# Optimization experiments

Measured on AMD Instinct MI355X. Metric: run time of the kernel, lower is better.

Reference implementation:

```python
import jax, jax.numpy as jnp
import numpy as np

N, E, G = 50000, 800000, 128
F_IN, H, NHID, C = 310, 128, 64, 2  # H = 2*nhid
NEG_SLOPE = 0.2


def setup_inputs() -> dict:
    key = jax.random.key(0)
    ks = jax.random.split(key, 16)
    def lin(k, fan_in, shape):
        return (jax.random.normal(k, shape, jnp.float32) / np.sqrt(fan_in)).astype(jnp.float32)
    return {
        "x": jax.random.normal(ks[0], (N, F_IN), jnp.float32),
        "edge_index": jax.random.randint(ks[1], (2, E), 0, N, dtype=jnp.int32),
        "batch": jnp.sort(jax.random.randint(ks[2], (N,), 0, G, dtype=jnp.int32)),
        "W1": lin(ks[3], F_IN, (F_IN, H)),
        "a_src1": lin(ks[4], H, (H,)),
        "a_dst1": lin(ks[5], H, (H,)),
        "b1": jnp.zeros((H,), jnp.float32),
        "W2": lin(ks[6], H, (H, H)),
        "a_src2": lin(ks[7], H, (H,)),
        "a_dst2": lin(ks[8], H, (H,)),
        "b2": jnp.zeros((H,), jnp.float32),
        "fc1_w": lin(ks[9], H, (H, NHID)),
        "fc1_b": jnp.zeros((NHID,), jnp.float32),
        "fc2_w": lin(ks[10], NHID, (NHID, C)),
        "fc2_b": jnp.zeros((C,), jnp.float32),
    }


def _gat(x, src, dst, W, a_src, a_dst, b):
    # PyG GATConv, heads=1: h = xW; e_ij = LeakyReLU(a_src.h_j + a_dst.h_i)
    h = x @ W                               # [N, H]
    asrc = h @ a_src                        # [N]
    adst = h @ a_dst                        # [N]
    e = jax.nn.leaky_relu(asrc[src] + adst[dst], NEG_SLOPE)  # [E']
    # segment softmax over incoming edges of each target node
    m = jax.ops.segment_max(e, dst, num_segments=N)
    ex = jnp.exp(e - m[dst])
    s = jax.ops.segment_sum(ex, dst, num_segments=N)
    w = ex / s[dst]                         # [E']
    out = jax.ops.segment_sum(h[src] * w[:, None], dst, num_segments=N)
    return out + b


def reference(x, edge_index, batch, W1, a_src1, a_dst1, b1,
              W2, a_src2, a_dst2, b2, fc1_w, fc1_b, fc2_w, fc2_b):
    # add self loops (GATConv default add_self_loops=True)
    ar = jnp.arange(N, dtype=edge_index.dtype)
    src = jnp.concatenate([edge_index[0], ar])
    dst = jnp.concatenate([edge_index[1], ar])

    h = jax.nn.selu(_gat(x, src, dst, W1, a_src1, a_dst1, b1))
    h = jax.nn.selu(_gat(h, src, dst, W2, a_src2, a_dst2, b2))

    # global mean pool over graphs
    summed = jax.ops.segment_sum(h, batch, num_segments=G)          # [G, H]
    cnt = jax.ops.segment_sum(jnp.ones((N,), h.dtype), batch, num_segments=G)
    pooled = jax.nn.selu(summed / jnp.maximum(cnt, 1.0)[:, None])

    z = jax.nn.selu(pooled @ fc1_w + fc1_b)  # dropout is identity in eval
    logits = z @ fc2_w + fc2_b
    return jax.nn.log_softmax(logits, axis=-1)
```

## Files before the change

kernel.cpp:

```cpp
#include <hip/hip_runtime.h>
#include <hip/hip_bf16.h>
#include <math.h>

#define NN 50000
#define NE 800000
#define NET (NE + NN)
#define FIN 310
#define HD 128
#define NHID 64
#define NCLS 2
#define NG 128
#define NEG_SLOPE 0.2f
#define KP1 320
#define KP2 128

#define SLOTS 64
#define NPART 8
#define PART_SZ (NN / NPART)
#define EPB 4096
#define NSLICE ((NET + EPB - 1) / EPB)

#define SELU_SCALE 1.0507009873554804934193349852946f
#define SELU_ALPHA 1.6732632423543772848170429916717f

typedef short bf16x8 __attribute__((ext_vector_type(8)));
typedef float f32x4 __attribute__((ext_vector_type(4)));

__device__ __forceinline__ float selu(float x) {
    return SELU_SCALE * (x > 0.f ? x : SELU_ALPHA * (__expf(x) - 1.f));
}
__device__ __forceinline__ float lrelu(float x) {
    return x > 0.f ? x : NEG_SLOPE * x;
}
__device__ __forceinline__ unsigned short f2bf(float f) {
    unsigned int u = __float_as_uint(f);
    u = (u + 0x7fffu + ((u >> 16) & 1u)) >> 16;
    return (unsigned short)u;
}
__device__ __forceinline__ float bf2f(unsigned short b) {
    return __uint_as_float(((unsigned int)b) << 16);
}


__global__ __launch_bounds__(256) void k_scatter_slots(const int* __restrict__ ei,
                                                       int* __restrict__ cursor,
                                                       int* __restrict__ slots) {
    int part = blockIdx.x & (NPART - 1);
    int slice = blockIdx.x >> 3;
    int lo = part * PART_SZ;
    int base = slice * EPB + threadIdx.x;
#pragma unroll
    for (int k = 0; k < EPB / 256; ++k) {
        int i = base + k * 256;
        if (i >= NET) break;
        int d = (i < NE) ? ei[NE + i] : (i - NE);
        if ((unsigned)(d - lo) < (unsigned)PART_SZ) {
            int s = (i < NE) ? ei[i] : d;
            int pos = atomicAdd(&cursor[d], 1) & (SLOTS - 1);
            slots[(size_t)d * SLOTS + pos] = s;
        }
    }
}


__global__ void k_castT2(const float* __restrict__ W1, const float* __restrict__ W2,
                         unsigned short* __restrict__ W1t, unsigned short* __restrict__ W2t) {
    int i = blockIdx.x * blockDim.x + threadIdx.x;
    const int N1 = HD * KP1;
    if (i < N1) {
        int n = i / KP1, k = i % KP1;
        W1t[i] = (k < FIN) ? f2bf(W1[(size_t)k * HD + n]) : (unsigned short)0;
    } else {
        int j = i - N1;
        if (j < HD * KP2) {
            int n = j / KP2, k = j % KP2;
            W2t[j] = f2bf(W2[(size_t)k * HD + n]);
        }
    }
}


#define GEMM_EPILOGUE                                                          \
    int rh = w & 1, chf = w >> 1;                                              \
    int gr_base = r0 + rh * 16 + quad * 4;                                     \
    _Pragma("unroll")                                                          \
    for (int r = 0; r < 4; ++r) {                                              \
        int gr = gr_base + r;                                                  \
        if (gr < M) {                                                          \
            _Pragma("unroll")                                                  \
            for (int nt = 0; nt < 4; ++nt)                                     \
                C[(size_t)gr * HD + chf * 64 + nt * 16 + l16] = f2bf(acc[nt][r]); \
        }                                                                      \
    }                                                                          \
    _Pragma("unroll")                                                          \
    for (int r = 0; r < 4; ++r) {                                              \
        float s1 = 0.f, s2 = 0.f;                                              \
        _Pragma("unroll")                                                      \
        for (int nt = 0; nt < 4; ++nt) {                                       \
            int c = chf * 64 + nt * 16 + l16;                                  \
            float v = acc[nt][r];                                              \
            s1 += v * a1s[c];                                                  \
            s2 += v * a2s[c];                                                  \
        }                                                                      \
        _Pragma("unroll")                                                      \
        for (int off = 1; off < 16; off <<= 1) {                               \
            s1 += __shfl_xor(s1, off);                                         \
            s2 += __shfl_xor(s2, off);                                         \
        }                                                                      \
        if (l16 == 0) {                                                        \
            pd[0][rh][chf][quad * 4 + r] = s1;                                 \
            pd[1][rh][chf][quad * 4 + r] = s2;                                 \
        }                                                                      \
    }                                                                          \
    __syncthreads();                                                           \
    if (t < 64) {                                                              \
        int idx = t & 15;                                                      \
        int rh2 = (t >> 4) & 1;                                                \
        int which = t >> 5;                                                    \
        float val = pd[which][rh2][0][idx] + pd[which][rh2][1][idx];           \
        int gr = r0 + rh2 * 16 + idx;                                          \
        if (gr < M) { if (which) adstp[gr] = val; else asrcp[gr] = val; }      \
    }

__global__ __launch_bounds__(256) void k_gemm_f32(const float* __restrict__ A,
                                                  const unsigned short* __restrict__ Bt,
                                                  unsigned short* __restrict__ C,
                                                  float* __restrict__ asrcp,
                                                  float* __restrict__ adstp,
                                                  const float* __restrict__ a_src,
                                                  const float* __restrict__ a_dst,
                                                  int M, int K, int Kp) {
    __shared__ unsigned short As[32][40];
    __shared__ unsigned short Bs[128][40];
    __shared__ float a1s[HD], a2s[HD];
    __shared__ float pd[2][2][2][16];
    int t = threadIdx.x;
    int lane = t & 63, w = t >> 6;
    int quad = lane >> 4, l16 = lane & 15;
    int r0 = blockIdx.x * 32;

    if (t < HD) a1s[t] = a_src[t];
    else a2s[t - HD] = a_dst[t - HD];

    f32x4 acc[4] = {};
    int arow = t >> 4;
    int acol = (t & 15) * 2;
    int brow = t >> 1;
    int bcol = (t & 1) * 16;

    for (int k0 = 0; k0 < Kp; k0 += 32) {
#pragma unroll
        for (int p = 0; p < 2; ++p) {
            int rl = arow + p * 16;
            int gr = r0 + rl;
            int gk = k0 + acol;
            float2 v = make_float2(0.f, 0.f);
            if (gr < M) {
                if (gk + 1 < K) v = *(const float2*)(A + (size_t)gr * K + gk);
                else if (gk < K) v.x = A[(size_t)gr * K + gk];
            }
            ushort2 b;
            b.x = f2bf(v.x); b.y = f2bf(v.y);
            *(ushort2*)&As[rl][acol] = b;
        }
        {
            const unsigned short* src = Bt + (size_t)brow * Kp + k0 + bcol;
            uint4 u0 = *(const uint4*)(src);
            uint4 u1 = *(const uint4*)(src + 8);
            *(uint4*)&Bs[brow][bcol] = u0;
            *(uint4*)&Bs[brow][bcol + 8] = u1;
        }
        __syncthreads();
        bf16x8 af = *(bf16x8*)&As[(w & 1) * 16 + l16][quad * 8];
#pragma unroll
        for (int nt = 0; nt < 4; ++nt) {
            bf16x8 bfr = *(bf16x8*)&Bs[(w >> 1) * 64 + nt * 16 + l16][quad * 8];
            acc[nt] = __builtin_amdgcn_mfma_f32_16x16x32_bf16(af, bfr, acc[nt], 0, 0, 0);
        }
        __syncthreads();
    }
    GEMM_EPILOGUE
}

__global__ __launch_bounds__(256) void k_gemm_bf16(const unsigned short* __restrict__ A,
                                                   const unsigned short* __restrict__ Bt,
                                                   unsigned short* __restrict__ C,
                                                   float* __restrict__ asrcp,
                                                   float* __restrict__ adstp,
                                                   const float* __restrict__ a_src,
                                                   const float* __restrict__ a_dst,
                                                   int M, int K, int Kp) {
    __shared__ unsigned short As[32][40];
    __shared__ unsigned short Bs[128][40];
    __shared__ float a1s[HD], a2s[HD];
    __shared__ float pd[2][2][2][16];
    int t = threadIdx.x;
    int lane = t & 63, w = t >> 6;
    int quad = lane >> 4, l16 = lane & 15;
    int r0 = blockIdx.x * 32;

    if (t < HD) a1s[t] = a_src[t];
    else a2s[t - HD] = a_dst[t - HD];

    f32x4 acc[4] = {};
    int arow = t >> 3;
    int acol = (t & 7) * 4;
    int brow = t >> 1;
    int bcol = (t & 1) * 16;

    for (int k0 = 0; k0 < Kp; k0 += 32) {
        {
            int gr = r0 + arow;
            uint2 v = make_uint2(0, 0);
            if (gr < M) v = *(const uint2*)(A + (size_t)gr * K + k0 + acol);
            *(uint2*)&As[arow][acol] = v;
        }
        {
            const unsigned short* src = Bt + (size_t)brow * Kp + k0 + bcol;
            uint4 u0 = *(const uint4*)(src);
            uint4 u1 = *(const uint4*)(src + 8);
            *(uint4*)&Bs[brow][bcol] = u0;
            *(uint4*)&Bs[brow][bcol + 8] = u1;
        }
        __syncthreads();
        bf16x8 af = *(bf16x8*)&As[(w & 1) * 16 + l16][quad * 8];
#pragma unroll
        for (int nt = 0; nt < 4; ++nt) {
            bf16x8 bfr = *(bf16x8*)&Bs[(w >> 1) * 64 + nt * 16 + l16][quad * 8];
            acc[nt] = __builtin_amdgcn_mfma_f32_16x16x32_bf16(af, bfr, acc[nt], 0, 0, 0);
        }
        __syncthreads();
    }
    GEMM_EPILOGUE
}


__global__ __launch_bounds__(256) void k_gat(const unsigned short* __restrict__ h,
                                             const float* __restrict__ asrc,
                                             const float* __restrict__ adst,
                                             const int* __restrict__ degv,
                                             const int* __restrict__ slots,
                                             const float* __restrict__ bias,
                                             unsigned short* __restrict__ out) {
    int node = blockIdx.x * 4 + (threadIdx.x >> 6);
    int lane = threadIdx.x & 63;
    if (node >= NN) return;
    int g = lane >> 4, cl = lane & 15;
    int deg = degv[node];
    float adsti = adst[node];

    float2 acc2[4] = {};

    int cnt = min(deg, SLOTS);
    int s_c = 0; float p_c = 0.f;
    if (lane < cnt) {
        s_c = slots[(size_t)node * SLOTS + lane];
        p_c = __expf(lrelu(asrc[s_c] + adsti));
    }
    float den_l = p_c;
    int nt = (cnt + 3) >> 2;
    for (int t = 0; t < nt; t += 2) {
        float pv[2]; uint4 hv[2];
#pragma unroll
        for (int u = 0; u < 2; ++u) {
            int tt = t + u;
            bool valid = tt < nt;
            int e = (4 * tt + g) & 63;
            int s = __shfl(s_c, e);
            float p = __shfl(p_c, e);
            int sa = valid ? s : 0;
            pv[u] = valid ? p : 0.f;
            hv[u] = *(const uint4*)(h + (size_t)sa * HD + cl * 8);
        }
#pragma unroll
        for (int u = 0; u < 2; ++u) {
            float p = pv[u];
            unsigned int w0 = hv[u].x, w1 = hv[u].y, w2 = hv[u].z, w3 = hv[u].w;
            acc2[0].x += p * __uint_as_float(w0 << 16);
            acc2[0].y += p * __uint_as_float(w0 & 0xffff0000u);
            acc2[1].x += p * __uint_as_float(w1 << 16);
            acc2[1].y += p * __uint_as_float(w1 & 0xffff0000u);
            acc2[2].x += p * __uint_as_float(w2 << 16);
            acc2[2].y += p * __uint_as_float(w2 & 0xffff0000u);
            acc2[3].x += p * __uint_as_float(w3 << 16);
            acc2[3].y += p * __uint_as_float(w3 & 0xffff0000u);
        }
    }
#pragma unroll
    for (int k = 0; k < 4; ++k) {
        acc2[k].x += __shfl_xor(acc2[k].x, 16);
        acc2[k].y += __shfl_xor(acc2[k].y, 16);
        acc2[k].x += __shfl_xor(acc2[k].x, 32);
        acc2[k].y += __shfl_xor(acc2[k].y, 32);
    }
#pragma unroll
    for (int off = 32; off; off >>= 1)
        den_l += __shfl_xor(den_l, off);

    if (g == 0) {
        float inv = 1.f / den_l;
        int c0 = cl * 8;
        float4 b0 = *(const float4*)(bias + c0);
        float4 b1 = *(const float4*)(bias + c0 + 4);
        float v0 = selu(acc2[0].x * inv + b0.x);
        float v1 = selu(acc2[0].y * inv + b0.y);
        float v2 = selu(acc2[1].x * inv + b0.z);
        float v3 = selu(acc2[1].y * inv + b0.w);
        float v4 = selu(acc2[2].x * inv + b1.x);
        float v5 = selu(acc2[2].y * inv + b1.y);
        float v6 = selu(acc2[3].x * inv + b1.z);
        float v7 = selu(acc2[3].y * inv + b1.w);
        uint4 pk;
        pk.x = (unsigned int)f2bf(v0) | ((unsigned int)f2bf(v1) << 16);
        pk.y = (unsigned int)f2bf(v2) | ((unsigned int)f2bf(v3) << 16);
        pk.z = (unsigned int)f2bf(v4) | ((unsigned int)f2bf(v5) << 16);
        pk.w = (unsigned int)f2bf(v6) | ((unsigned int)f2bf(v7) << 16);
        *(uint4*)(out + (size_t)node * HD + c0) = pk;
    }
}


__device__ __forceinline__ int lower_bound_i(const int* a, int n, int key) {
    int lo = 0, hi = n;
    while (lo < hi) {
        int mid = (lo + hi) >> 1;
        if (a[mid] < key) lo = mid + 1; else hi = mid;
    }
    return lo;
}

__global__ __launch_bounds__(512) void k_poolfc(const unsigned short* __restrict__ x,
                                                const int* __restrict__ batch,
                                                const float* __restrict__ w1,
                                                const float* __restrict__ b1,
                                                const float* __restrict__ w2,
                                                const float* __restrict__ b2,
                                                float* __restrict__ out) {
    int g = blockIdx.x;
    int t = threadIdx.x;
    __shared__ int lo_s, hi_s;
    __shared__ float red[512];
    __shared__ float pooled_s[128];
    if (t == 0) {
        lo_s = lower_bound_i(batch, NN, g);
        hi_s = lower_bound_i(batch, NN, g + 1);
    }
    __syncthreads();
    int lo = lo_s, hi = hi_s;
    float acc = 0.f;
    for (int n = lo + (t >> 7); n < hi; n += 4)
        acc += bf2f(x[(size_t)n * HD + (t & 127)]);
    red[t] = acc;
    __syncthreads();
    if (t < 128) {
        float v = red[t] + red[t + 128] + red[t + 256] + red[t + 384];
        pooled_s[t] = selu(v / fmaxf((float)(hi - lo), 1.f));
    }
    __syncthreads();
    if (t < 64) {
        float z = 0.f;
#pragma unroll 8
        for (int k = 0; k < HD; ++k) z += pooled_s[k] * w1[k * NHID + t];
        z = selu(z + b1[t]);
        float p0 = z * w2[t * NCLS + 0];
        float p1 = z * w2[t * NCLS + 1];
        for (int off = 32; off; off >>= 1) {
            p0 += __shfl_down(p0, off);
            p1 += __shfl_down(p1, off);
        }
        if (t == 0) {
            float l0 = p0 + b2[0], l1 = p1 + b2[1];
            float m = fmaxf(l0, l1);
            float lse = m + __logf(__expf(l0 - m) + __expf(l1 - m));
            out[g * NCLS + 0] = l0 - lse;
            out[g * NCLS + 1] = l1 - lse;
        }
    }
}


static inline size_t align_up(size_t v, size_t a) { return (v + a - 1) / a * a; }

extern "C" void kernel_launch(void* const* d_in, const int* in_sizes, int n_in,
                              void* d_out, int out_size, void* d_ws, size_t ws_size,
                              hipStream_t stream) {
    const float* x      = (const float*)d_in[0];
    const int*   ei     = (const int*)d_in[1];
    const int*   batch  = (const int*)d_in[2];
    const float* W1     = (const float*)d_in[3];
    const float* a_src1 = (const float*)d_in[4];
    const float* a_dst1 = (const float*)d_in[5];
    const float* b1     = (const float*)d_in[6];
    const float* W2     = (const float*)d_in[7];
    const float* a_src2 = (const float*)d_in[8];
    const float* a_dst2 = (const float*)d_in[9];
    const float* b2     = (const float*)d_in[10];
    const float* fc1_w  = (const float*)d_in[11];
    const float* fc1_b  = (const float*)d_in[12];
    const float* fc2_w  = (const float*)d_in[13];
    const float* fc2_b  = (const float*)d_in[14];
    float* out = (float*)d_out;

    char* ws = (char*)d_ws;
    size_t off = 0;
    unsigned short* h1 = (unsigned short*)(ws + off); off = align_up(off + (size_t)NN * HD * 2, 256);
    unsigned short* o1 = (unsigned short*)(ws + off); off = align_up(off + (size_t)NN * HD * 2, 256);
    float* asrc = (float*)(ws + off); off = align_up(off + (size_t)NN * 4, 256);
    float* adst = (float*)(ws + off); off = align_up(off + (size_t)NN * 4, 256);
    int* cursor = (int*)(ws + off);   off = align_up(off + (size_t)NN * 4, 256);
    int* slots  = (int*)(ws + off);   off = align_up(off + (size_t)NN * SLOTS * 4, 256);
    unsigned short* W1t = (unsigned short*)(ws + off); off = align_up(off + (size_t)HD * KP1 * 2, 256);
    unsigned short* W2t = (unsigned short*)(ws + off); off = align_up(off + (size_t)HD * KP2 * 2, 256);
    (void)ws_size;

    hipMemsetAsync(cursor, 0, (size_t)NN * 4, stream);
    k_scatter_slots<<<NSLICE * NPART, 256, 0, stream>>>(ei, cursor, slots);

    k_castT2<<<(HD * (KP1 + KP2) + 255) / 256, 256, 0, stream>>>(W1, W2, W1t, W2t);

    int gblocks = (NN + 31) / 32;

    k_gemm_f32<<<gblocks, 256, 0, stream>>>(x, W1t, h1, asrc, adst, a_src1, a_dst1, NN, FIN, KP1);
    k_gat<<<(NN + 3) / 4, 256, 0, stream>>>(h1, asrc, adst, cursor, slots, b1, o1);

    k_gemm_bf16<<<gblocks, 256, 0, stream>>>(o1, W2t, h1, asrc, adst, a_src2, a_dst2, NN, HD, KP2);
    k_gat<<<(NN + 3) / 4, 256, 0, stream>>>(h1, asrc, adst, cursor, slots, b2, o1);

    k_poolfc<<<NG, 512, 0, stream>>>(o1, batch, fc1_w, fc1_b, fc2_w, fc2_b, out);
}
```

Baseline: 309.1 us.

## Rewrite GEMMs to read pre-cast bf16 operands directly from global memory without LDS

Adds a separate pass that casts x to padded bf16 and repacks the weights into an MFMA-fragment-friendly layout. The two GEMM kernels are merged into one templated kernel that loads A and B fragments straight from global memory, with no shared-memory staging or barriers, and computes 64 rows by 128 columns per block. It also shrinks the slot-list indices from int to 16-bit. The new cast pass adds an extra write and read of x, and the 16-bit indices cannot hold node ids of 65536 or more, but NN is 50000.

New measurement: 314.1 us. Within noise of the previous version (+1.6%).

```diff
diff --git a/kernel.cpp b/kernel.cpp
--- a/kernel.cpp
+++ b/kernel.cpp
@@ -44,7 +44,7 @@
 
 __global__ __launch_bounds__(256) void k_scatter_slots(const int* __restrict__ ei,
                                                        int* __restrict__ cursor,
-                                                       int* __restrict__ slots) {
+                                                       unsigned short* __restrict__ slots) {
     int part = blockIdx.x & (NPART - 1);
     int slice = blockIdx.x >> 3;
     int lo = part * PART_SZ;
@@ -57,181 +57,103 @@
         if ((unsigned)(d - lo) < (unsigned)PART_SZ) {
             int s = (i < NE) ? ei[i] : d;
             int pos = atomicAdd(&cursor[d], 1) & (SLOTS - 1);
-            slots[(size_t)d * SLOTS + pos] = s;
-        }
-    }
-}
-
-
-__global__ void k_castT2(const float* __restrict__ W1, const float* __restrict__ W2,
-                         unsigned short* __restrict__ W1t, unsigned short* __restrict__ W2t) {
+            slots[(size_t)d * SLOTS + pos] = (unsigned short)s;
+        }
+    }
+}
+
+
+__global__ __launch_bounds__(256) void k_castx(const float* __restrict__ x,
+                                               unsigned short* __restrict__ xbf) {
+    int i = blockIdx.x * blockDim.x + threadIdx.x;
+    if (i >= NN * (KP1 / 2)) return;
+    int row = i / (KP1 / 2);
+    int kk = (i % (KP1 / 2)) * 2;
+    unsigned int pk = 0;
+    if (kk + 1 < FIN) {
+        float2 v = *(const float2*)(x + (size_t)row * FIN + kk);
+        pk = (unsigned int)f2bf(v.x) | ((unsigned int)f2bf(v.y) << 16);
+    }
+    *(unsigned int*)(xbf + (size_t)row * KP1 + kk) = pk;
+}
+
+
+__global__ void k_castW(const float* __restrict__ W1, const float* __restrict__ W2,
+                        unsigned short* __restrict__ W1p, unsigned short* __restrict__ W2p) {
     int i = blockIdx.x * blockDim.x + threadIdx.x;
     const int N1 = HD * KP1;
     if (i < N1) {
         int n = i / KP1, k = i % KP1;
-        W1t[i] = (k < FIN) ? f2bf(W1[(size_t)k * HD + n]) : (unsigned short)0;
+        unsigned short v = (k < FIN) ? f2bf(W1[(size_t)k * HD + n]) : (unsigned short)0;
+        W1p[((k >> 3) * HD + n) * 8 + (k & 7)] = v;
     } else {
         int j = i - N1;
         if (j < HD * KP2) {
             int n = j / KP2, k = j % KP2;
-            W2t[j] = f2bf(W2[(size_t)k * HD + n]);
-        }
-    }
-}
-
-
-#define GEMM_EPILOGUE                                                          \
-    int rh = w & 1, chf = w >> 1;                                              \
-    int gr_base = r0 + rh * 16 + quad * 4;                                     \
-    _Pragma("unroll")                                                          \
-    for (int r = 0; r < 4; ++r) {                                              \
-        int gr = gr_base + r;                                                  \
-        if (gr < M) {                                                          \
-            _Pragma("unroll")                                                  \
-            for (int nt = 0; nt < 4; ++nt)                                     \
-                C[(size_t)gr * HD + chf * 64 + nt * 16 + l16] = f2bf(acc[nt][r]); \
-        }                                                                      \
-    }                                                                          \
-    _Pragma("unroll")                                                          \
-    for (int r = 0; r < 4; ++r) {                                              \
-        float s1 = 0.f, s2 = 0.f;                                              \
-        _Pragma("unroll")                                                      \
-        for (int nt = 0; nt < 4; ++nt) {                                       \
-            int c = chf * 64 + nt * 16 + l16;                                  \
-            float v = acc[nt][r];                                              \
-            s1 += v * a1s[c];                                                  \
-            s2 += v * a2s[c];                                                  \
-        }                                                                      \
-        _Pragma("unroll")                                                      \
-        for (int off = 1; off < 16; off <<= 1) {                               \
-            s1 += __shfl_xor(s1, off);                                         \
-            s2 += __shfl_xor(s2, off);                                         \
-        }                                                                      \
-        if (l16 == 0) {                                                        \
-            pd[0][rh][chf][quad * 4 + r] = s1;                                 \
-            pd[1][rh][chf][quad * 4 + r] = s2;                                 \
-        }                                                                      \
-    }                                                                          \
-    __syncthreads();                                                           \
-    if (t < 64) {                                                              \
-        int idx = t & 15;                                                      \
-        int rh2 = (t >> 4) & 1;                                                \
-        int which = t >> 5;                                                    \
-        float val = pd[which][rh2][0][idx] + pd[which][rh2][1][idx];           \
-        int gr = r0 + rh2 * 16 + idx;                                          \
-        if (gr < M) { if (which) adstp[gr] = val; else asrcp[gr] = val; }      \
-    }
-
-__global__ __launch_bounds__(256) void k_gemm_f32(const float* __restrict__ A,
-                                                  const unsigned short* __restrict__ Bt,
-                                                  unsigned short* __restrict__ C,
-                                                  float* __restrict__ asrcp,
-                                                  float* __restrict__ adstp,
-                                                  const float* __restrict__ a_src,
-                                                  const float* __restrict__ a_dst,
-                                                  int M, int K, int Kp) {
-    __shared__ unsigned short As[32][40];
-    __shared__ unsigned short Bs[128][40];
-    __shared__ float a1s[HD], a2s[HD];
-    __shared__ float pd[2][2][2][16];
+            W2p[((k >> 3) * HD + n) * 8 + (k & 7)] = f2bf(W2[(size_t)k * HD + n]);
+        }
+    }
+}
+
+
+template <int KP>
+__global__ __launch_bounds__(256) void k_gemm(const unsigned short* __restrict__ A,
+                                              const unsigned short* __restrict__ Bp,
+                                              unsigned short* __restrict__ C,
+                                              float* __restrict__ asrcp,
+                                              float* __restrict__ adstp,
+                                              const float* __restrict__ a_src,
+                                              const float* __restrict__ a_dst,
+                                              int M) {
     int t = threadIdx.x;
     int lane = t & 63, w = t >> 6;
     int quad = lane >> 4, l16 = lane & 15;
-    int r0 = blockIdx.x * 32;
-
-    if (t < HD) a1s[t] = a_src[t];
-    else a2s[t - HD] = a_dst[t - HD];
-
-    f32x4 acc[4] = {};
-    int arow = t >> 4;
-    int acol = (t & 15) * 2;
-    int brow = t >> 1;
-    int bcol = (t & 1) * 16;
-
-    for (int k0 = 0; k0 < Kp; k0 += 32) {
-#pragma unroll
-        for (int p = 0; p < 2; ++p) {
-            int rl = arow + p * 16;
-            int gr = r0 + rl;
-            int gk = k0 + acol;
-            float2 v = make_float2(0.f, 0.f);
-            if (gr < M) {
-                if (gk + 1 < K) v = *(const float2*)(A + (size_t)gr * K + gk);
-                else if (gk < K) v.x = A[(size_t)gr * K + gk];
-            }
-            ushort2 b;
-            b.x = f2bf(v.x); b.y = f2bf(v.y);
-            *(ushort2*)&As[rl][acol] = b;
-        }
-        {
-            const unsigned short* src = Bt + (size_t)brow * Kp + k0 + bcol;
-            uint4 u0 = *(const uint4*)(src);
-            uint4 u1 = *(const uint4*)(src + 8);
-            *(uint4*)&Bs[brow][bcol] = u0;
-            *(uint4*)&Bs[brow][bcol + 8] = u1;
-        }
-        __syncthreads();
-        bf16x8 af = *(bf16x8*)&As[(w & 1) * 16 + l16][quad * 8];
-#pragma unroll
-        for (int nt = 0; nt < 4; ++nt) {
-            bf16x8 bfr = *(bf16x8*)&Bs[(w >> 1) * 64 + nt * 16 + l16][quad * 8];
+    int r0 = blockIdx.x * 64;
+
+    int grow = r0 + w * 16 + l16;
+    int arow = min(grow, M - 1);
+    const unsigned short* aptr = A + (size_t)arow * KP + quad * 8;
+
+    f32x4 acc[8] = {};
+#pragma unroll 2
+    for (int k0 = 0; k0 < KP; k0 += 32) {
+        bf16x8 af = *(const bf16x8*)(aptr + k0);
+        const unsigned short* bbase = Bp + ((size_t)(k0 >> 3) + quad) * (HD * 8) + l16 * 8;
+#pragma unroll
+        for (int nt = 0; nt < 8; ++nt) {
+            bf16x8 bfr = *(const bf16x8*)(bbase + nt * 128);
             acc[nt] = __builtin_amdgcn_mfma_f32_16x16x32_bf16(af, bfr, acc[nt], 0, 0, 0);
         }
-        __syncthreads();
-    }
-    GEMM_EPILOGUE
-}
-
-__global__ __launch_bounds__(256) void k_gemm_bf16(const unsigned short* __restrict__ A,
-                                                   const unsigned short* __restrict__ Bt,
-                                                   unsigned short* __restrict__ C,
-                                                   float* __restrict__ asrcp,
-                                                   float* __restrict__ adstp,
-                                                   const float* __restrict__ a_src,
-                                                   const float* __restrict__ a_dst,
-                                                   int M, int K, int Kp) {
-    __shared__ unsigned short As[32][40];
-    __shared__ unsigned short Bs[128][40];
-    __shared__ float a1s[HD], a2s[HD];
-    __shared__ float pd[2][2][2][16];
-    int t = threadIdx.x;
-    int lane = t & 63, w = t >> 6;
-    int quad = lane >> 4, l16 = lane & 15;
-    int r0 = blockIdx.x * 32;
-
-    if (t < HD) a1s[t] = a_src[t];
-    else a2s[t - HD] = a_dst[t - HD];
-
-    f32x4 acc[4] = {};
-    int arow = t >> 3;
-    int acol = (t & 7) * 4;
-    int brow = t >> 1;
-    int bcol = (t & 1) * 16;
-
-    for (int k0 = 0; k0 < Kp; k0 += 32) {
-        {
-            int gr = r0 + arow;
-            uint2 v = make_uint2(0, 0);
-            if (gr < M) v = *(const uint2*)(A + (size_t)gr * K + k0 + acol);
-            *(uint2*)&As[arow][acol] = v;
-        }
-        {
-            const unsigned short* src = Bt + (size_t)brow * Kp + k0 + bcol;
-            uint4 u0 = *(const uint4*)(src);
-            uint4 u1 = *(const uint4*)(src + 8);
-            *(uint4*)&Bs[brow][bcol] = u0;
-            *(uint4*)&Bs[brow][bcol + 8] = u1;
-        }
-        __syncthreads();
-        bf16x8 af = *(bf16x8*)&As[(w & 1) * 16 + l16][quad * 8];
-#pragma unroll
-        for (int nt = 0; nt < 4; ++nt) {
-            bf16x8 bfr = *(bf16x8*)&Bs[(w >> 1) * 64 + nt * 16 + l16][quad * 8];
-            acc[nt] = __builtin_amdgcn_mfma_f32_16x16x32_bf16(af, bfr, acc[nt], 0, 0, 0);
-        }
-        __syncthreads();
-    }
-    GEMM_EPILOGUE
+    }
+
+    int gr_base = r0 + w * 16 + quad * 4;
+#pragma unroll
+    for (int r = 0; r < 4; ++r) {
+        int gr = gr_base + r;
+        if (gr < M) {
+#pragma unroll
+            for (int nt = 0; nt < 8; ++nt)
+                C[(size_t)gr * HD + nt * 16 + l16] = f2bf(acc[nt][r]);
+        }
+    }
+#pragma unroll
+    for (int r = 0; r < 4; ++r) {
+        float s1 = 0.f, s2 = 0.f;
+#pragma unroll
+        for (int nt = 0; nt < 8; ++nt) {
+            int c = nt * 16 + l16;
+            float v = acc[nt][r];
+            s1 += v * a_src[c];
+            s2 += v * a_dst[c];
+        }
+#pragma unroll
+        for (int off = 1; off < 16; off <<= 1) {
+            s1 += __shfl_xor(s1, off);
+            s2 += __shfl_xor(s2, off);
+        }
+        int gr = gr_base + r;
+        if (l16 == 0 && gr < M) { asrcp[gr] = s1; adstp[gr] = s2; }
+    }
 }
 
 
@@ -239,7 +161,7 @@
                                              const float* __restrict__ asrc,
                                              const float* __restrict__ adst,
                                              const int* __restrict__ degv,
-                                             const int* __restrict__ slots,
+                                             const unsigned short* __restrict__ slots,
                                              const float* __restrict__ bias,
                                              unsigned short* __restrict__ out) {
     int node = blockIdx.x * 4 + (threadIdx.x >> 6);
@@ -403,27 +325,29 @@
 
     char* ws = (char*)d_ws;
     size_t off = 0;
-    unsigned short* h1 = (unsigned short*)(ws + off); off = align_up(off + (size_t)NN * HD * 2, 256);
-    unsigned short* o1 = (unsigned short*)(ws + off); off = align_up(off + (size_t)NN * HD * 2, 256);
+    unsigned short* xbf = (unsigned short*)(ws + off); off = align_up(off + (size_t)NN * KP1 * 2, 256);
+    unsigned short* h1  = (unsigned short*)(ws + off); off = align_up(off + (size_t)NN * HD * 2, 256);
+    unsigned short* o1  = (unsigned short*)(ws + off); off = align_up(off + (size_t)NN * HD * 2, 256);
     float* asrc = (float*)(ws + off); off = align_up(off + (size_t)NN * 4, 256);
     float* adst = (float*)(ws + off); off = align_up(off + (size_t)NN * 4, 256);
     int* cursor = (int*)(ws + off);   off = align_up(off + (size_t)NN * 4, 256);
-    int* slots  = (int*)(ws + off);   off = align_up(off + (size_t)NN * SLOTS * 4, 256);
-    unsigned short* W1t = (unsigned short*)(ws + off); off = align_up(off + (size_t)HD * KP1 * 2, 256);
-    unsigned short* W2t = (unsigned short*)(ws + off); off = align_up(off + (size_t)HD * KP2 * 2, 256);
+    unsigned short* slots = (unsigned short*)(ws + off); off = align_up(off + (size_t)NN * SLOTS * 2, 256);
+    unsigned short* W1p = (unsigned short*)(ws + off); off = align_up(off + (size_t)HD * KP1 * 2, 256);
+    unsigned short* W2p = (unsigned short*)(ws + off); off = align_up(off + (size_t)HD * KP2 * 2, 256);
     (void)ws_size;
 
     hipMemsetAsync(cursor, 0, (size_t)NN * 4, stream);
     k_scatter_slots<<<NSLICE * NPART, 256, 0, stream>>>(ei, cursor, slots);
 
-    k_castT2<<<(HD * (KP1 + KP2) + 255) / 256, 256, 0, stream>>>(W1, W2, W1t, W2t);
-
-    int gblocks = (NN + 31) / 32;
-
-    k_gemm_f32<<<gblocks, 256, 0, stream>>>(x, W1t, h1, asrc, adst, a_src1, a_dst1, NN, FIN, KP1);
+    k_castx<<<(NN * (KP1 / 2) + 255) / 256, 256, 0, stream>>>(x, xbf);
+    k_castW<<<(HD * (KP1 + KP2) + 255) / 256, 256, 0, stream>>>(W1, W2, W1p, W2p);
+
+    int gblocks = (NN + 63) / 64;
+
+    k_gemm<KP1><<<gblocks, 256, 0, stream>>>(xbf, W1p, h1, asrc, adst, a_src1, a_dst1, NN);
     k_gat<<<(NN + 3) / 4, 256, 0, stream>>>(h1, asrc, adst, cursor, slots, b1, o1);
 
-    k_gemm_bf16<<<gblocks, 256, 0, stream>>>(o1, W2t, h1, asrc, adst, a_src2, a_dst2, NN, HD, KP2);
+    k_gemm<KP2><<<gblocks, 256, 0, stream>>>(o1, W2p, h1, asrc, adst, a_src2, a_dst2, NN);
     k_gat<<<(NN + 3) / 4, 256, 0, stream>>>(h1, asrc, adst, cursor, slots, b2, o1);
 
     k_poolfc<<<NG, 512, 0, stream>>>(o1, batch, fc1_w, fc1_b, fc2_w, fc2_b, out);
```
